# Kernel optimization log

Hardware: AMD Instinct MI355X
Metric: run time of the kernel (lower is better)

The kernel has to match this reference:

```python
import jax, jax.numpy as jnp
import numpy as np

N = 40000      # input points
M = 40000      # output points
E = 500000     # flat neighbor edges (ragged flattened)
F = 32         # input feature channels
C = 64         # output channels
K = 15         # kernel points
EXTENT = 0.6


def _make_kernel_points(k, radius):
    # Deterministic stand-in for load_kernels(): first point fixed at center,
    # remaining points spread inside a ball of the given radius.
    rng = np.random.RandomState(0)
    pts = rng.randn(k, 3).astype(np.float32)
    pts /= np.linalg.norm(pts, axis=1, keepdims=True) + 1e-9
    scale = rng.rand(k, 1).astype(np.float32) ** (1.0 / 3.0)
    pts = pts * scale * radius
    pts[0] = 0.0  # fixed='center'
    return jnp.asarray(pts)


def setup_inputs() -> dict:
    key = jax.random.key(0)
    ks = jax.random.split(key, 6)
    points = jax.random.uniform(ks[0], (N, 3), dtype=jnp.float32)
    features = jax.random.normal(ks[1], (N, F), dtype=jnp.float32)
    output_points = jax.random.uniform(ks[2], (M, 3), dtype=jnp.float32)
    neighbor_indices = jax.random.randint(ks[3], (E,), 0, N, dtype=jnp.int32)
    segment_ids = jnp.sort(jax.random.randint(ks[4], (E,), 0, M, dtype=jnp.int32))
    k_points = _make_kernel_points(K, 1.5 * EXTENT)          # [K,3] constant
    k_values = jax.random.normal(ks[5], (K, F, C), dtype=jnp.float32) * 0.05
    return {
        "points": points,
        "features": features,
        "output_points": output_points,
        "neighbor_indices": neighbor_indices,
        "segment_ids": segment_ids,
        "k_points": k_points,
        "k_values": k_values,
    }


def reference(points, features, output_points, neighbor_indices, segment_ids,
              k_points, k_values):
    # Gather neighbor coords/features and recenter around each output point.
    rel = points[neighbor_indices] - output_points[segment_ids]      # [E,3]
    nbr_feat = features[neighbor_indices]                            # [E,F]

    # Per-kernel-point squared distances and linear influence weights.
    diff = rel[:, None, :] - k_points[None, :, :]                    # [E,K,3]
    sq_dist = jnp.sum(diff * diff, axis=-1)                          # [E,K]
    w = jnp.maximum(1.0 - jnp.sqrt(sq_dist) / EXTENT, 0.0)           # [E,K]

    # Weighted features and ragged segment-sum per output point.
    weighted = w[:, :, None] * nbr_feat[:, None, :]                  # [E,K,F]
    agg = jax.ops.segment_sum(weighted, segment_ids, num_segments=M,
                              indices_are_sorted=True)               # [M,K,F]

    # Batched matmul over kernel points, then sum over kernel points.
    out = jnp.einsum('mkf,kfc->mc', agg, k_values)                   # [M,C]
    return out
```

## Files before the change

### kernel.cpp

```cpp
#include <hip/hip_runtime.h>

typedef __attribute__((ext_vector_type(8))) short bf16x8;
typedef __attribute__((ext_vector_type(8))) _Float16 f16x8;
typedef __attribute__((ext_vector_type(4))) float f32x4;
typedef __attribute__((ext_vector_type(4))) _Float16 f16x4;
typedef __attribute__((ext_vector_type(2))) _Float16 f16x2;

#define NPTS   40000
#define MOUT   40000
#define EDG    500000
#define FIN    32
#define COUT   64
#define KP     15
#define KFDIM  (KP * FIN)
#define EXTENT 0.6f

#define FSTRIDE 112
#define WSTRIDE 40
#define WAVE_LDS (16 * FSTRIDE + 16 * WSTRIDE)
#define ASTR 488
#define SEGB 8

#define FEAT_BLKS  (NPTS * FIN / 1024)
#define PTS_BLKS   ((NPTS + 255) / 256)
#define OP_BLKS    ((MOUT + 255) / 256)
#define ROW_BLKS   ((EDG + 255) / 256)
#define WT_BLKS    (KFDIM * COUT / 256)
#define PRE_BLKS   (FEAT_BLKS + PTS_BLKS + OP_BLKS + ROW_BLKS + WT_BLKS)

__device__ __forceinline__ short f2bf(float x) {
    union { float f; unsigned u; } v; v.f = x;
    unsigned r = (v.u + 0x7fffu + ((v.u >> 16) & 1u)) >> 16;
    return (short)r;
}

__global__ __launch_bounds__(256) void preprocess_all(
    const float* __restrict__ features, _Float16* __restrict__ feat_i,
    const float* __restrict__ pts, float4* __restrict__ p4,
    const float* __restrict__ opts, float4* __restrict__ op4,
    const int* __restrict__ seg_ids, int* __restrict__ row_start,
    const float* __restrict__ k_values, _Float16* __restrict__ w_t)
{
    const int bid = blockIdx.x;
    if (bid < FEAT_BLKS) {
        const int d0 = (bid * 256 + threadIdx.x) * 4;
        #pragma unroll
        for (int u = 0; u < 4; ++u) {
            const int d = d0 + u;
            const int p = d >> 5, q = d & 31;
            const int fp = q >> 1, h = q & 1;
            feat_i[d] = (_Float16)features[p * FIN + fp + 16 * h];
        }
    } else if (bid < FEAT_BLKS + PTS_BLKS) {
        const int i = (bid - FEAT_BLKS) * 256 + threadIdx.x;
        if (i < NPTS) {
            const float* p = pts + 3 * i;
            p4[i] = make_float4(p[0], p[1], p[2], 0.f);
        }
    } else if (bid < FEAT_BLKS + PTS_BLKS + OP_BLKS) {
        const int i = (bid - FEAT_BLKS - PTS_BLKS) * 256 + threadIdx.x;
        if (i < MOUT) {
            const float* p = opts + 3 * i;
            op4[i] = make_float4(p[0], p[1], p[2], 0.f);
        }
    } else if (bid < FEAT_BLKS + PTS_BLKS + OP_BLKS + ROW_BLKS) {
        const int e = (bid - FEAT_BLKS - PTS_BLKS - OP_BLKS) * 256 + threadIdx.x;
        if (e >= EDG) return;
        const int cur  = seg_ids[e];
        const int prev = (e == 0) ? -1 : seg_ids[e - 1];
        for (int m = prev + 1; m <= cur; ++m) row_start[m] = e;
        if (e == EDG - 1)
            for (int m = cur + 1; m <= MOUT; ++m) row_start[m] = EDG;
    } else {
        const int d = (bid - FEAT_BLKS - PTS_BLKS - OP_BLKS - ROW_BLKS) * 256
                      + threadIdx.x;
        const int c = d / KFDIM, r = d % KFDIM;
        const int k = r >> 5, q = r & 31;
        const int fp = q >> 1, h = q & 1;
        w_t[d] = (_Float16)k_values[(k * FIN + fp + 16 * h) * COUT + c];
    }
}

__global__ __launch_bounds__(256, 5) void kpconv_fused2(
    const float4* __restrict__ points4,
    const _Float16* __restrict__ feat_i,
    const float4* __restrict__ op4,
    const int*   __restrict__ nbr_idx,
    const int*   __restrict__ row_start,
    const float* __restrict__ k_points,
    const _Float16* __restrict__ w_t,
    float* __restrict__ out)
{
    __shared__ __align__(16) _Float16 aggT[16 * ASTR];
    __shared__ __align__(16) unsigned char stage[4 * WAVE_LDS];

    const int tid  = threadIdx.x;
    const int wave = tid >> 6;
    const int lane = tid & 63;
    const int quad = lane >> 4;
    const int l16  = lane & 15;
    const int esl  = lane >> 2;
    const int kg   = lane & 3;
    const int m0   = blockIdx.x * SEGB;

    unsigned char* fbase = stage + wave * WAVE_LDS;
    unsigned char* wbase = fbase + 16 * FSTRIDE;

    float kx[4], ky[4], kz[4];
    #pragma unroll
    for (int t = 0; t < 4; ++t) {
        const int k  = kg * 4 + t;
        const int kk = k < KP ? k : 0;
        kx[t] = k_points[kk * 3 + 0];
        ky[t] = k_points[kk * 3 + 1];
        kz[t] = k_points[kk * 3 + 2];
    }
    const float inv_ext = 1.f / EXTENT;

    int rs[3];
    #pragma unroll
    for (int i = 0; i < 3; ++i) rs[i] = row_start[m0 + wave * 2 + i];

    int nstart[2];
    nstart[1] = rs[2];
    nstart[0] = (rs[1] < rs[2]) ? rs[1] : rs[2];
    const int fstart = (rs[0] < rs[1]) ? rs[0] : nstart[0];

    int wb = -0x40000000;
    int nbrreg = 0;
    uint4  fc_n = {0, 0, 0, 0};
    float4 p_n  = make_float4(0.f, 0.f, 0.f, 0.f);

    auto pref = [&](int es) {
        if (es + 15 > wb + 63) {
            wb = es;
            const int a = wb + lane;
            nbrreg = nbr_idx[a < EDG ? a : EDG - 1];
        }
        const int e  = es + esl;
        const int nb = __shfl(nbrreg, e - wb);
        fc_n = *(const uint4*)(feat_i + nb * FIN + kg * 8);
        p_n  = ((const float4*)points4)[nb];
    };

    pref(fstart);

    #pragma unroll
    for (int j = 0; j < 2; ++j) {
        const int e0 = rs[j];
        const int e1 = rs[j + 1];
        const float4 o = op4[m0 + wave * 2 + j];

        f32x4 c_lo = {0.f, 0.f, 0.f, 0.f};
        f32x4 c_hi = {0.f, 0.f, 0.f, 0.f};

        for (int es = e0; es < e1; es += 16) {
            const uint4  fc = fc_n;
            const float4 p  = p_n;
            const int nes = (es + 16 < e1) ? es + 16 : nstart[j];
            pref(nes);

            *(uint4*)(fbase + esl * FSTRIDE + kg * 16) = fc;

            const float rx = p.x - o.x, ry = p.y - o.y, rz = p.z - o.z;
            const bool evalid = (es + esl) < e1;
            #pragma unroll
            for (int t = 0; t < 4; ++t) {
                const float dx = rx - kx[t], dy = ry - ky[t], dz = rz - kz[t];
                float w = 1.f - sqrtf(dx * dx + dy * dy + dz * dz) * inv_ext;
                w = w > 0.f ? w : 0.f;
                if (!evalid || (kg * 4 + t) >= KP) w = 0.f;
                *(_Float16*)(wbase + (kg * 4 + t) * WSTRIDE + esl * 2) = (_Float16)w;
            }

            const f16x4 af = *(const f16x4*)(wbase + l16 * WSTRIDE + quad * 8);
            f16x2 w2[4];
            #pragma unroll
            for (int jj = 0; jj < 4; ++jj)
                w2[jj] = *(const f16x2*)(fbase + (quad * 4 + jj) * FSTRIDE + l16 * 4);
            const f16x4 blo = {w2[0][0], w2[1][0], w2[2][0], w2[3][0]};
            const f16x4 bhi = {w2[0][1], w2[1][1], w2[2][1], w2[3][1]};

            c_lo = __builtin_amdgcn_mfma_f32_16x16x16f16(af, blo, c_lo, 0, 0, 0);
            c_hi = __builtin_amdgcn_mfma_f32_16x16x16f16(af, bhi, c_hi, 0, 0, 0);
        }

        _Float16* dst = aggT + (wave * 2 + j) * ASTR;
        #pragma unroll
        for (int r = 0; r < 4; ++r) {
            const int krow = quad * 4 + r;
            if (krow < KP) {
                f16x2 v = {(_Float16)c_lo[r], (_Float16)c_hi[r]};
                *(f16x2*)(dst + krow * 32 + 2 * l16) = v;
            }
        }
    }

    __syncthreads();

    const int bcol = wave * 16 + l16;
    const _Float16* wrow = w_t + (size_t)bcol * KFDIM + quad * 8;
    const _Float16* arow = aggT + l16 * ASTR + quad * 8;

    f32x4 c = {0.f, 0.f, 0.f, 0.f};
    #pragma unroll
    for (int s = 0; s < 15; ++s) {
        const f16x8 a = *(const f16x8*)(arow + 32 * s);
        const f16x8 b = *(const f16x8*)(wrow + 32 * s);
        c = __builtin_amdgcn_mfma_f32_16x16x32_f16(a, b, c, 0, 0, 0);
    }

    #pragma unroll
    for (int r = 0; r < 4; ++r) {
        const int seg = quad * 4 + r;
        if (seg < SEGB)
            out[(m0 + seg) * COUT + bcol] = c[r];
    }
}

__global__ __launch_bounds__(256, 4) void kpconv_agg_fallback(
    const float* __restrict__ points,
    const float* __restrict__ features,
    const float* __restrict__ output_points,
    const int*   __restrict__ nbr_idx,
    const int*   __restrict__ seg_ids,
    const float* __restrict__ k_points,
    _Float16* __restrict__ agg_g)
{
    __shared__ int seg_start[5];

    const int tid = threadIdx.x;
    const int m0  = blockIdx.x * 4;

    if (tid <= 4) {
        const int target = m0 + tid;
        int lo = 0, hi = EDG;
        while (lo < hi) {
            int mid = (lo + hi) >> 1;
            if (seg_ids[mid] < target) lo = mid + 1; else hi = mid;
        }
        seg_start[tid] = lo;
    }
    __syncthreads();

    const int wave = tid >> 6;
    const int lane = tid & 63;
    const int quad = lane >> 4;
    const int l16  = lane & 15;

    const int m = m0 + wave;
    const float ox = output_points[m * 3 + 0];
    const float oy = output_points[m * 3 + 1];
    const float oz = output_points[m * 3 + 2];

    const int myk = l16 < KP ? l16 : 0;
    const float kpx = k_points[myk * 3 + 0];
    const float kpy = k_points[myk * 3 + 1];
    const float kpz = k_points[myk * 3 + 2];
    const float inv_ext = 1.f / EXTENT;

    const int e0 = seg_start[wave], e1 = seg_start[wave + 1];

    f32x4 c_lo = {0.f, 0.f, 0.f, 0.f};
    f32x4 c_hi = {0.f, 0.f, 0.f, 0.f};

    for (int es = e0; es < e1; es += 32) {
        const int last = e1 - 1;
        const int ebase = es + quad * 8;

        int nb[8];
        #pragma unroll
        for (int j = 0; j < 8; ++j) {
            const int e = ebase + j;
            nb[j] = nbr_idx[e < e1 ? e : last];
        }

        bf16x8 afrag, blo, bhi;
        #pragma unroll
        for (int j = 0; j < 8; ++j) {
            const float* pp = points + nb[j] * 3;
            const float rx = pp[0] - ox;
            const float ry = pp[1] - oy;
            const float rz = pp[2] - oz;
            const float dx = rx - kpx, dy = ry - kpy, dz = rz - kpz;
            const float d2 = dx * dx + dy * dy + dz * dz;
            float w = 1.f - sqrtf(d2) * inv_ext;
            w = w > 0.f ? w : 0.f;
            if (l16 >= KP || ebase + j >= e1) w = 0.f;
            afrag[j] = f2bf(w);
        }

        #pragma unroll
        for (int j = 0; j < 8; ++j) {
            const float* fp = features + nb[j] * FIN + l16;
            blo[j] = f2bf(fp[0]);
            bhi[j] = f2bf(fp[16]);
        }

        c_lo = __builtin_amdgcn_mfma_f32_16x16x32_bf16(afrag, blo, c_lo, 0, 0, 0);
        c_hi = __builtin_amdgcn_mfma_f32_16x16x32_bf16(afrag, bhi, c_hi, 0, 0, 0);
    }

    _Float16* dst = agg_g + (size_t)m * KFDIM;
    #pragma unroll
    for (int r = 0; r < 4; ++r) {
        const int krow = quad * 4 + r;
        if (krow < KP) {
            dst[krow * FIN + l16]      = (_Float16)c_lo[r];
            dst[krow * FIN + 16 + l16] = (_Float16)c_hi[r];
        }
    }
}

__global__ __launch_bounds__(256, 4) void kpconv_gemm_plain(
    const _Float16* __restrict__ agg_g,
    const float* __restrict__ k_values,
    float* __restrict__ out)
{
    const int tid  = threadIdx.x;
    const int wave = tid >> 6;
    const int lane = tid & 63;
    const int quad = lane >> 4;
    const int l16  = lane & 15;
    const int m0   = blockIdx.x * 32;
    const int bcol = wave * 16 + l16;

    f16x8 bfr[15];
    #pragma unroll
    for (int s = 0; s < 15; ++s) {
        #pragma unroll
        for (int j = 0; j < 8; ++j)
            bfr[s][j] = (_Float16)k_values[(32 * s + quad * 8 + j) * COUT + bcol];
    }

    const _Float16* arow0 = agg_g + (size_t)(m0 + l16) * KFDIM + quad * 8;
    const _Float16* arow1 = arow0 + 16 * KFDIM;

    f32x4 c0 = {0.f, 0.f, 0.f, 0.f};
    f32x4 c1 = {0.f, 0.f, 0.f, 0.f};
    #pragma unroll
    for (int s = 0; s < 15; ++s) {
        const f16x8 a0 = *(const f16x8*)(arow0 + 32 * s);
        const f16x8 a1 = *(const f16x8*)(arow1 + 32 * s);
        c0 = __builtin_amdgcn_mfma_f32_16x16x32_f16(a0, bfr[s], c0, 0, 0, 0);
        c1 = __builtin_amdgcn_mfma_f32_16x16x32_f16(a1, bfr[s], c1, 0, 0, 0);
    }

    #pragma unroll
    for (int r = 0; r < 4; ++r) {
        out[(m0 + quad * 4 + r) * COUT + bcol]      = c0[r];
        out[(m0 + 16 + quad * 4 + r) * COUT + bcol] = c1[r];
    }
}

extern "C" void kernel_launch(void* const* d_in, const int* in_sizes, int n_in,
                              void* d_out, int out_size, void* d_ws, size_t ws_size,
                              hipStream_t stream) {
    const float* points        = (const float*)d_in[0];
    const float* features      = (const float*)d_in[1];
    const float* output_points = (const float*)d_in[2];
    const int*   nbr_idx       = (const int*)d_in[3];
    const int*   seg_ids       = (const int*)d_in[4];
    const float* k_points      = (const float*)d_in[5];
    const float* k_values      = (const float*)d_in[6];
    float* out = (float*)d_out;

    const size_t feat_bytes = (size_t)NPTS * FIN * sizeof(_Float16);
    const size_t pts4_bytes = (size_t)NPTS * sizeof(float4);
    const size_t op4_bytes  = (size_t)MOUT * sizeof(float4);
    const size_t rs_bytes   = ((size_t)(MOUT + 1) * sizeof(int) + 15) & ~15ul;
    const size_t wt_bytes   = (size_t)KFDIM * COUT * sizeof(_Float16);
    const size_t full_bytes = feat_bytes + pts4_bytes + op4_bytes + rs_bytes
                            + wt_bytes;

    if (ws_size >= full_bytes) {
        char* p = (char*)d_ws;
        _Float16* feat_i    = (_Float16*)p;  p += feat_bytes;
        float4*   points4   = (float4*)p;    p += pts4_bytes;
        float4*   op4       = (float4*)p;    p += op4_bytes;
        int*      row_start = (int*)p;       p += rs_bytes;
        _Float16* w_t       = (_Float16*)p;

        preprocess_all<<<PRE_BLKS, 256, 0, stream>>>(
            features, feat_i, points, points4, output_points, op4,
            seg_ids, row_start, k_values, w_t);
        kpconv_fused2<<<MOUT / SEGB, 256, 0, stream>>>(
            points4, feat_i, op4, nbr_idx, row_start, k_points, w_t, out);
    } else {
        _Float16* agg_g = (_Float16*)d_ws;
        kpconv_agg_fallback<<<MOUT / 4, 256, 0, stream>>>(
            points, features, output_points, nbr_idx, seg_ids, k_points, agg_g);
        kpconv_gemm_plain<<<MOUT / 32, 256, 0, stream>>>(agg_g, k_values, out);
    }
}
```

Measured before the change: 112.4 us.

## Process 32 output segments per block, 8 per wave, two MFMA tiles in matmul

Each block now handles 32 output points instead of 8, with each wave aggregating 8 segments rather than 2. The final matmul fills a full 32-row aggregate tile, so every weight row loaded from global memory feeds two MFMAs. The earlier 8-row block wasted half of each 16-row MFMA tile. This cuts redundant weight traffic and per-block overhead, but it leaves 4x fewer blocks, enlarges LDS use, and lowers the occupancy target from 5 to 4, so latency hiding and load balance may suffer.

```diff
diff --git a/kernel.cpp b/kernel.cpp
--- a/kernel.cpp
+++ b/kernel.cpp
@@ -19,7 +19,8 @@
 #define WSTRIDE 40
 #define WAVE_LDS (16 * FSTRIDE + 16 * WSTRIDE)
 #define ASTR 488
-#define SEGB 8
+#define SEGW 8
+#define SEGB 32
 
 #define FEAT_BLKS  (NPTS * FIN / 1024)
 #define PTS_BLKS   ((NPTS + 255) / 256)
@@ -81,7 +82,7 @@
     }
 }
 
-__global__ __launch_bounds__(256, 5) void kpconv_fused2(
+__global__ __launch_bounds__(256, 4) void kpconv_fused2(
     const float4* __restrict__ points4,
     const _Float16* __restrict__ feat_i,
     const float4* __restrict__ op4,
@@ -91,7 +92,7 @@
     const _Float16* __restrict__ w_t,
     float* __restrict__ out)
 {
-    __shared__ __align__(16) _Float16 aggT[16 * ASTR];
+    __shared__ __align__(16) _Float16 aggT[SEGB * ASTR];
     __shared__ __align__(16) unsigned char stage[4 * WAVE_LDS];
 
     const int tid  = threadIdx.x;
@@ -117,13 +118,15 @@
     }
     const float inv_ext = 1.f / EXTENT;
 
-    int rs[3];
-    #pragma unroll
-    for (int i = 0; i < 3; ++i) rs[i] = row_start[m0 + wave * 2 + i];
-
-    int nstart[2];
-    nstart[1] = rs[2];
-    nstart[0] = (rs[1] < rs[2]) ? rs[1] : rs[2];
+    int rs[SEGW + 1];
+    #pragma unroll
+    for (int i = 0; i <= SEGW; ++i) rs[i] = row_start[m0 + wave * SEGW + i];
+
+    int nstart[SEGW];
+    nstart[SEGW - 1] = rs[SEGW];
+    #pragma unroll
+    for (int i = SEGW - 2; i >= 0; --i)
+        nstart[i] = (rs[i + 1] < rs[i + 2]) ? rs[i + 1] : nstart[i + 1];
     const int fstart = (rs[0] < rs[1]) ? rs[0] : nstart[0];
 
     int wb = -0x40000000;
@@ -146,10 +149,10 @@
     pref(fstart);
 
     #pragma unroll
-    for (int j = 0; j < 2; ++j) {
+    for (int j = 0; j < SEGW; ++j) {
         const int e0 = rs[j];
         const int e1 = rs[j + 1];
-        const float4 o = op4[m0 + wave * 2 + j];
+        const float4 o = op4[m0 + wave * SEGW + j];
 
         f32x4 c_lo = {0.f, 0.f, 0.f, 0.f};
         f32x4 c_hi = {0.f, 0.f, 0.f, 0.f};
@@ -185,7 +188,7 @@
             c_hi = __builtin_amdgcn_mfma_f32_16x16x16f16(af, bhi, c_hi, 0, 0, 0);
         }
 
-        _Float16* dst = aggT + (wave * 2 + j) * ASTR;
+        _Float16* dst = aggT + (wave * SEGW + j) * ASTR;
         #pragma unroll
         for (int r = 0; r < 4; ++r) {
             const int krow = quad * 4 + r;
@@ -199,22 +202,25 @@
     __syncthreads();
 
     const int bcol = wave * 16 + l16;
-    const _Float16* wrow = w_t + (size_t)bcol * KFDIM + quad * 8;
-    const _Float16* arow = aggT + l16 * ASTR + quad * 8;
-
-    f32x4 c = {0.f, 0.f, 0.f, 0.f};
+    const _Float16* wrow  = w_t + (size_t)bcol * KFDIM + quad * 8;
+    const _Float16* arow0 = aggT + l16 * ASTR + quad * 8;
+    const _Float16* arow1 = aggT + (16 + l16) * ASTR + quad * 8;
+
+    f32x4 c0 = {0.f, 0.f, 0.f, 0.f};
+    f32x4 c1 = {0.f, 0.f, 0.f, 0.f};
     #pragma unroll
     for (int s = 0; s < 15; ++s) {
-        const f16x8 a = *(const f16x8*)(arow + 32 * s);
-        const f16x8 b = *(const f16x8*)(wrow + 32 * s);
-        c = __builtin_amdgcn_mfma_f32_16x16x32_f16(a, b, c, 0, 0, 0);
+        const f16x8 b  = *(const f16x8*)(wrow + 32 * s);
+        const f16x8 a0 = *(const f16x8*)(arow0 + 32 * s);
+        const f16x8 a1 = *(const f16x8*)(arow1 + 32 * s);
+        c0 = __builtin_amdgcn_mfma_f32_16x16x32_f16(a0, b, c0, 0, 0, 0);
+        c1 = __builtin_amdgcn_mfma_f32_16x16x32_f16(a1, b, c1, 0, 0, 0);
     }
 
     #pragma unroll
     for (int r = 0; r < 4; ++r) {
-        const int seg = quad * 4 + r;
-        if (seg < SEGB)
-            out[(m0 + seg) * COUT + bcol] = c[r];
+        out[(m0 + quad * 4 + r) * COUT + bcol]      = c0[r];
+        out[(m0 + 16 + quad * 4 + r) * COUT + bcol] = c1[r];
     }
 }
 
```

Result: faster. 102.4 us (-8.9%).
